# Performance work log

Hardware: AMD Instinct MI355X
Metric: run time of the kernel (lower is better)

The kernel has to match this reference:

```python
import jax, jax.numpy as jnp
import numpy as np


def setup_inputs() -> dict:
    key = jax.random.key(0)
    ks = jax.random.split(key, 8)
    n_videos, emb_dim = 200000, 128
    n_nodes, k_neigh = 20000, 32
    sc = 1.0 / np.sqrt(emb_dim)
    return {
        "video_embeddings": jax.random.normal(ks[0], (n_videos, emb_dim), jnp.float32),
        "video_nodes": jax.random.randint(ks[1], (n_nodes,), 0, n_videos, jnp.int64 if jax.config.jax_enable_x64 else jnp.int32),
        "neigh_idx": jax.random.randint(ks[2], (n_nodes, k_neigh), 0, n_videos, jnp.int64 if jax.config.jax_enable_x64 else jnp.int32),
        "W1": jax.random.normal(ks[3], (2 * emb_dim, emb_dim), jnp.float32) * sc,
        "b1": jnp.zeros((emb_dim,), jnp.float32),
        "W2": jax.random.normal(ks[4], (emb_dim, emb_dim), jnp.float32) * sc,
        "b2": jnp.zeros((emb_dim,), jnp.float32),
        "W3": jax.random.normal(ks[5], (emb_dim, 1), jnp.float32) * sc,
        "b3": jnp.zeros((1,), jnp.float32),
    }


def reference(video_embeddings, video_nodes, neigh_idx, W1, b1, W2, b2, W3, b3):
    # Ragged per-node loop vectorized as a padded [N, K] neighbor gather.
    neigh_emb = video_embeddings[neigh_idx]          # [N, K, D]
    node_emb = video_embeddings[video_nodes]         # [N, D]
    n, k, d = neigh_emb.shape
    # Attention MLP: cat(neigh, node_repeated) -> relu -> relu -> scalar score
    x = jnp.concatenate([neigh_emb, jnp.broadcast_to(node_emb[:, None, :], (n, k, d))], axis=-1)  # [N, K, 2D]
    h = jax.nn.relu(jnp.einsum("nke,ed->nkd", x, W1) + b1)
    h = jax.nn.relu(jnp.einsum("nke,ed->nkd", h, W2) + b2)
    scores = (jnp.einsum("nkd,do->nko", h, W3) + b3)[..., 0]  # [N, K]
    att = jax.nn.softmax(scores, axis=-1)                      # softmax over neighbors
    # Weighted aggregation: embed_matrix[i] = neigh_emb[i].T @ att[i]
    return jnp.einsum("nkd,nk->nd", neigh_emb, att)
```

## Files before the change

### kernel.cpp

```cpp
#include <hip/hip_runtime.h>
#include <hip/hip_bf16.h>

#define D  128
#define KN 32

typedef __attribute__((ext_vector_type(8))) short bf16x8;
typedef __attribute__((ext_vector_type(4))) float f32x4;

static __device__ __forceinline__ unsigned short f2bf(float f) {
    union { float f; unsigned int u; } v; v.f = f;
    unsigned int u = v.u;
    u += 0x7fff + ((u >> 16) & 1);
    return (unsigned short)(u >> 16);
}
static __device__ __forceinline__ float bf2f(unsigned short h) {
    union { float f; unsigned int u; } v; v.u = ((unsigned int)h) << 16;
    return v.f;
}

__global__ __launch_bounds__(256) void wt_kernel(
    const float* __restrict__ W1, const float* __restrict__ W2,
    unsigned short* __restrict__ W1Tt, unsigned short* __restrict__ W1Tb,
    unsigned short* __restrict__ W2T)
{
    int idx = blockIdx.x * 256 + threadIdx.x;
    if (idx < D * D) {
        int col = idx >> 7, e = idx & 127;
        W1Tt[col * D + e] = f2bf(W1[e * D + col]);
        W1Tb[col * D + e] = f2bf(W1[(D + e) * D + col]);
        W2T [col * D + e] = f2bf(W2[e * D + col]);
    }
}

__global__ __launch_bounds__(256) void p1q_kernel(
    const float* __restrict__ emb, const int* __restrict__ vnodes,
    int NV, int NN, int nvBlocks,
    const unsigned short* __restrict__ W1Tt, const unsigned short* __restrict__ W1Tb,
    const float* __restrict__ b1,
    unsigned short* __restrict__ P1, unsigned short* __restrict__ Q,
    unsigned short* __restrict__ EB)
{
    __shared__ unsigned short sA[128][136];

    const int tid  = threadIdx.x;
    const int lane = tid & 63;
    const int w    = tid >> 6;
    const int m    = lane & 15, q = lane >> 4;

    const bool nv = (int)blockIdx.x < nvBlocks;
    const int  bi = nv ? blockIdx.x : blockIdx.x - nvBlocks;
    const int  M  = nv ? NV : NN;
    const unsigned short* WT = nv ? W1Tt : W1Tb;
    unsigned short* dst = nv ? P1 : Q;
    const int r0 = bi * 128;

#pragma unroll
    for (int i = 0; i < 16; ++i) {
        int e = tid + 256 * i;
        int row = e >> 5, c4 = (e & 31) << 2;
        int r = r0 + row; if (r > M - 1) r = M - 1;
        int vr = nv ? r : vnodes[r];
        const float4 f = *(const float4*)(emb + (long)vr * D + c4);
        ushort4 h;
        h.x = f2bf(f.x); h.y = f2bf(f.y); h.z = f2bf(f.z); h.w = f2bf(f.w);
        *(ushort4*)(&sA[row][c4]) = h;
    }
    __syncthreads();

    if (nv) {
        int row = tid >> 1, half = tid & 1;
        if (r0 + row < M) {
#pragma unroll
            for (int j = 0; j < 8; ++j)
                *(bf16x8*)(EB + (long)(r0 + row) * D + half * 64 + j * 8) =
                    *(const bf16x8*)(&sA[row][half * 64 + j * 8]);
        }
    }

    bf16x8 Bf[2][4];
#pragma unroll
    for (int nt = 0; nt < 2; ++nt)
#pragma unroll
        for (int kk = 0; kk < 4; ++kk)
            Bf[nt][kk] = *(const bf16x8*)(WT + (32 * w + 16 * nt + m) * D + kk * 32 + q * 8);
    float bv[2];
#pragma unroll
    for (int nt = 0; nt < 2; ++nt) bv[nt] = nv ? 0.f : b1[32 * w + 16 * nt + m];

    f32x4 acc[8][2];
#pragma unroll
    for (int mt = 0; mt < 8; ++mt)
#pragma unroll
        for (int nt = 0; nt < 2; ++nt) acc[mt][nt] = (f32x4){0.f, 0.f, 0.f, 0.f};

#pragma unroll
    for (int kk = 0; kk < 4; ++kk) {
#pragma unroll
        for (int mt = 0; mt < 8; ++mt) {
            bf16x8 a = *(const bf16x8*)(&sA[16 * mt + m][kk * 32 + q * 8]);
            acc[mt][0] = __builtin_amdgcn_mfma_f32_16x16x32_bf16(a, Bf[0][kk], acc[mt][0], 0, 0, 0);
            acc[mt][1] = __builtin_amdgcn_mfma_f32_16x16x32_bf16(a, Bf[1][kk], acc[mt][1], 0, 0, 0);
        }
    }

#pragma unroll
    for (int mt = 0; mt < 8; ++mt)
#pragma unroll
        for (int nt = 0; nt < 2; ++nt) {
            int col = 32 * w + 16 * nt + m;
#pragma unroll
            for (int r = 0; r < 4; ++r) {
                int row = r0 + 16 * mt + 4 * q + r;
                if (row < M) dst[(long)row * D + col] = f2bf(acc[mt][nt][r] + bv[nt]);
            }
        }
}

__global__ __launch_bounds__(256, 2) void agg_kernel(
    const unsigned short* __restrict__ EB, const int* __restrict__ nidx,
    const unsigned short* __restrict__ W2T, const float* __restrict__ b2,
    const float* __restrict__ W3, const float* __restrict__ b3,
    const unsigned short* __restrict__ P1, const unsigned short* __restrict__ Q,
    float* __restrict__ out, int NN)
{
    __shared__ unsigned short sX[128][136];
    __shared__ int   sIdx[128];
    __shared__ float sSp[4][128];
    __shared__ float sAtt[128];

    const int tid  = threadIdx.x;
    const int lane = tid & 63;
    const int w    = tid >> 6;
    const int m    = lane & 15, q = lane >> 4;
    const int row  = tid >> 1, half = tid & 1;

    bf16x8 Bf[2][4];
#pragma unroll
    for (int nt = 0; nt < 2; ++nt)
#pragma unroll
        for (int kk = 0; kk < 4; ++kk)
            Bf[nt][kk] = *(const bf16x8*)(W2T + (32 * w + 16 * nt + m) * D + kk * 32 + q * 8);
    float b2v[2], w3v[2];
#pragma unroll
    for (int nt = 0; nt < 2; ++nt) {
        int col = 32 * w + 16 * nt + m;
        b2v[nt] = b2[col];
        w3v[nt] = W3[col];
    }
    const float b3s = b3[0];

    const int groups = (NN + 3) >> 2;

    int g = blockIdx.x;
    int ni_cur = 0;
    bf16x8 pf[8];
    if (g < groups) {
        int nd = g * 4 + (row >> 5); if (nd > NN - 1) nd = NN - 1;
        ni_cur = nidx[nd * KN + (row & 31)];
#pragma unroll
        for (int j = 0; j < 8; ++j)
            pf[j] = *(const bf16x8*)(P1 + (long)ni_cur * D + half * 64 + j * 8);
    }

    for (; g < groups; g += gridDim.x) {
        const int node0 = g * 4;
        int nd = node0 + (row >> 5); if (nd > NN - 1) nd = NN - 1;

        if (half == 0) sIdx[row] = ni_cur;
        {
            const bf16x8* qq = (const bf16x8*)(Q + (long)nd * D) + half * 8;
#pragma unroll
            for (int j = 0; j < 8; ++j) {
                bf16x8 qv = qq[j], r;
#pragma unroll
                for (int h = 0; h < 8; ++h) {
                    float v = bf2f((unsigned short)pf[j][h]) + bf2f((unsigned short)qv[h]);
                    r[h] = (short)f2bf(v > 0.f ? v : 0.f);
                }
                *(bf16x8*)(&sX[row][half * 64 + j * 8]) = r;
            }
        }

        const int gn = g + gridDim.x;
        const bool more = gn < groups;
        int ni_next = ni_cur;
        if (more) {
            int ndn = gn * 4 + (row >> 5); if (ndn > NN - 1) ndn = NN - 1;
            ni_next = nidx[ndn * KN + (row & 31)];
        }
        __syncthreads();

        bf16x8 gv[8];
#pragma unroll
        for (int j = 0; j < 8; ++j) {
            int k = (lane >> 4) + 4 * j;
            int ik = sIdx[w * KN + k];
            gv[j] = *(const bf16x8*)(EB + (long)ik * D + (lane & 15) * 8);
        }

        if (more) {
#pragma unroll
            for (int j = 0; j < 8; ++j)
                pf[j] = *(const bf16x8*)(P1 + (long)ni_next * D + half * 64 + j * 8);
        }

        f32x4 acc[8][2];
#pragma unroll
        for (int mt = 0; mt < 8; ++mt)
#pragma unroll
            for (int nt = 0; nt < 2; ++nt) acc[mt][nt] = (f32x4){0.f, 0.f, 0.f, 0.f};

#pragma unroll
        for (int kk = 0; kk < 4; ++kk) {
#pragma unroll
            for (int mt = 0; mt < 8; ++mt) {
                bf16x8 a = *(const bf16x8*)(&sX[16 * mt + m][kk * 32 + q * 8]);
                acc[mt][0] = __builtin_amdgcn_mfma_f32_16x16x32_bf16(a, Bf[0][kk], acc[mt][0], 0, 0, 0);
                acc[mt][1] = __builtin_amdgcn_mfma_f32_16x16x32_bf16(a, Bf[1][kk], acc[mt][1], 0, 0, 0);
            }
        }

#pragma unroll
        for (int mt = 0; mt < 8; ++mt) {
            float p[4];
#pragma unroll
            for (int r = 0; r < 4; ++r) {
                float h0 = acc[mt][0][r] + b2v[0]; h0 = h0 > 0.f ? h0 : 0.f;
                float h1 = acc[mt][1][r] + b2v[1]; h1 = h1 > 0.f ? h1 : 0.f;
                p[r] = h0 * w3v[0] + h1 * w3v[1];
            }
#pragma unroll
            for (int off = 8; off >= 1; off >>= 1)
#pragma unroll
                for (int r = 0; r < 4; ++r) p[r] += __shfl_xor(p[r], off, 16);
            if (m == 0) {
#pragma unroll
                for (int r = 0; r < 4; ++r) sSp[w][16 * mt + 4 * q + r] = p[r];
            }
        }
        __syncthreads();

        if (tid < 128) {
            float s = sSp[0][tid] + sSp[1][tid] + sSp[2][tid] + sSp[3][tid] + b3s;
            float mx = s;
#pragma unroll
            for (int off = 16; off >= 1; off >>= 1) mx = fmaxf(mx, __shfl_xor(mx, off, 32));
            float e = __expf(s - mx);
            float sum = e;
#pragma unroll
            for (int off = 16; off >= 1; off >>= 1) sum += __shfl_xor(sum, off, 32);
            sAtt[tid] = e / sum;
        }
        __syncthreads();

        {
            float r[8] = {0.f, 0.f, 0.f, 0.f, 0.f, 0.f, 0.f, 0.f};
#pragma unroll
            for (int j = 0; j < 8; ++j) {
                float a = sAtt[w * KN + (lane >> 4) + 4 * j];
#pragma unroll
                for (int h = 0; h < 8; ++h)
                    r[h] += a * bf2f((unsigned short)gv[j][h]);
            }
#pragma unroll
            for (int h = 0; h < 8; ++h) {
                r[h] += __shfl_xor(r[h], 16);
                r[h] += __shfl_xor(r[h], 32);
            }
            int ndw = node0 + w;
            if (lane < 16 && ndw < NN) {
                float4 o0 = {r[0], r[1], r[2], r[3]};
                float4 o1 = {r[4], r[5], r[6], r[7]};
                *(float4*)(out + (long)ndw * D + lane * 8)     = o0;
                *(float4*)(out + (long)ndw * D + lane * 8 + 4) = o1;
            }
        }
        ni_cur = ni_next;
    }
}

__global__ __launch_bounds__(128) void naive_kernel(
    const float* __restrict__ emb, const int* __restrict__ vnodes,
    const int* __restrict__ nidx,
    const float* __restrict__ W1, const float* __restrict__ b1,
    const float* __restrict__ W2, const float* __restrict__ b2,
    const float* __restrict__ W3, const float* __restrict__ b3,
    float* __restrict__ out)
{
    __shared__ float sE[KN + 1][D];
    __shared__ float sH[KN][D];
    __shared__ float sH2[KN][D];
    __shared__ float sS[KN];
    __shared__ float sA2[KN];
    const int node = blockIdx.x, tid = threadIdx.x;

    for (int r = 0; r < KN + 1; ++r) {
        int vr = (r < KN) ? nidx[node * KN + r] : vnodes[node];
        sE[r][tid] = emb[(long)vr * D + tid];
    }
    __syncthreads();
    for (int k = 0; k < KN; ++k) {
        float s = b1[tid];
        for (int e = 0; e < D; ++e) s += sE[k][e]  * W1[e * D + tid];
        for (int e = 0; e < D; ++e) s += sE[KN][e] * W1[(D + e) * D + tid];
        sH[k][tid] = s > 0.f ? s : 0.f;
    }
    __syncthreads();
    for (int k = 0; k < KN; ++k) {
        float s = b2[tid];
        for (int e = 0; e < D; ++e) s += sH[k][e] * W2[e * D + tid];
        sH2[k][tid] = s > 0.f ? s : 0.f;
    }
    __syncthreads();
    if (tid < KN) {
        float s = b3[0];
        for (int e = 0; e < D; ++e) s += sH2[tid][e] * W3[e];
        sS[tid] = s;
    }
    __syncthreads();
    if (tid == 0) {
        float mx = sS[0];
        for (int k = 1; k < KN; ++k) mx = fmaxf(mx, sS[k]);
        float sum = 0.f;
        for (int k = 0; k < KN; ++k) { sA2[k] = __expf(sS[k] - mx); sum += sA2[k]; }
        for (int k = 0; k < KN; ++k) sA2[k] /= sum;
    }
    __syncthreads();
    float a = 0.f;
    for (int k = 0; k < KN; ++k) a += sA2[k] * sE[k][tid];
    out[(long)node * D + tid] = a;
}

extern "C" void kernel_launch(void* const* d_in, const int* in_sizes, int n_in,
                              void* d_out, int out_size, void* d_ws, size_t ws_size,
                              hipStream_t stream) {
    const float* emb    = (const float*)d_in[0];
    const int*   vnodes = (const int*)d_in[1];
    const int*   nidx   = (const int*)d_in[2];
    const float* W1     = (const float*)d_in[3];
    const float* b1     = (const float*)d_in[4];
    const float* W2     = (const float*)d_in[5];
    const float* b2     = (const float*)d_in[6];
    const float* W3     = (const float*)d_in[7];
    const float* b3     = (const float*)d_in[8];
    float* out = (float*)d_out;

    const int NV = in_sizes[0] / D;
    const int NN = in_sizes[1];

    const size_t p1_elems = (size_t)NV * D;
    const size_t q_elems  = (size_t)NN * D;
    const size_t wt_elems = (size_t)D * D;
    const size_t need = (2 * p1_elems + q_elems + 3 * wt_elems) * sizeof(unsigned short);

    if (ws_size >= need) {
        unsigned short* P1   = (unsigned short*)d_ws;
        unsigned short* Q    = P1 + p1_elems;
        unsigned short* W1Tt = Q + q_elems;
        unsigned short* W1Tb = W1Tt + wt_elems;
        unsigned short* W2T  = W1Tb + wt_elems;
        unsigned short* EB   = W2T + wt_elems;

        const int nvBlocks = (NV + 127) / 128;
        const int qBlocks  = (NN + 127) / 128;

        wt_kernel<<<(D * D + 255) / 256, 256, 0, stream>>>(W1, W2, W1Tt, W1Tb, W2T);
        p1q_kernel<<<nvBlocks + qBlocks, 256, 0, stream>>>(
            emb, vnodes, NV, NN, nvBlocks, W1Tt, W1Tb, b1, P1, Q, EB);
        agg_kernel<<<1024, 256, 0, stream>>>(
            EB, nidx, W2T, b2, W3, b3, P1, Q, out, NN);
    } else {
        naive_kernel<<<NN, D, 0, stream>>>(emb, vnodes, nidx, W1, b1, W2, b2, W3, b3, out);
    }
}
```

Measured before the change: 302.7 us.

## Interleave P1 and bf16 embeddings per row, one-wave-per-node aggregation kernel

The precomputed W1 projection (P1) and the bf16 embedding copy now sit interleaved in a single 256-wide row, so each neighbour gather reads one contiguous 512-byte row instead of two separate buffers. The p1q output is staged through shared memory so global stores are coalesced. The aggregation kernel is restructured so each wave handles one node on its own: A fragments are built in registers, W2 lives in LDS, and scores and softmax are reduced with shuffles, which removes the block-wide barriers. Occupancy is raised to 4 blocks per SM, but the explicit prefetch of the next group's data is dropped.

Result: slower. 526.0 us (+73.8%).

```diff
diff --git a/kernel.cpp b/kernel.cpp
--- a/kernel.cpp
+++ b/kernel.cpp
@@ -37,8 +37,7 @@
     int NV, int NN, int nvBlocks,
     const unsigned short* __restrict__ W1Tt, const unsigned short* __restrict__ W1Tb,
     const float* __restrict__ b1,
-    unsigned short* __restrict__ P1, unsigned short* __restrict__ Q,
-    unsigned short* __restrict__ EB)
+    unsigned short* __restrict__ PE, unsigned short* __restrict__ Q)
 {
     __shared__ unsigned short sA[128][136];
 
@@ -51,7 +50,6 @@
     const int  bi = nv ? blockIdx.x : blockIdx.x - nvBlocks;
     const int  M  = nv ? NV : NN;
     const unsigned short* WT = nv ? W1Tt : W1Tb;
-    unsigned short* dst = nv ? P1 : Q;
     const int r0 = bi * 128;
 
 #pragma unroll
@@ -72,7 +70,7 @@
         if (r0 + row < M) {
 #pragma unroll
             for (int j = 0; j < 8; ++j)
-                *(bf16x8*)(EB + (long)(r0 + row) * D + half * 64 + j * 8) =
+                *(bf16x8*)(PE + (long)(r0 + row) * 256 + 128 + half * 64 + j * 8) =
                     *(const bf16x8*)(&sA[row][half * 64 + j * 8]);
         }
     }
@@ -103,179 +101,171 @@
         }
     }
 
+    __syncthreads();
 #pragma unroll
     for (int mt = 0; mt < 8; ++mt)
 #pragma unroll
         for (int nt = 0; nt < 2; ++nt) {
             int col = 32 * w + 16 * nt + m;
 #pragma unroll
-            for (int r = 0; r < 4; ++r) {
-                int row = r0 + 16 * mt + 4 * q + r;
-                if (row < M) dst[(long)row * D + col] = f2bf(acc[mt][nt][r] + bv[nt]);
+            for (int r = 0; r < 4; ++r)
+                sA[16 * mt + 4 * q + r][col] = f2bf(acc[mt][nt][r] + bv[nt]);
+        }
+    __syncthreads();
+    {
+        int row = tid >> 1, half = tid & 1;
+        int gr = r0 + row;
+        if (gr < M) {
+            if (nv) {
+#pragma unroll
+                for (int j = 0; j < 8; ++j)
+                    *(bf16x8*)(PE + (long)gr * 256 + half * 64 + j * 8) =
+                        *(const bf16x8*)(&sA[row][half * 64 + j * 8]);
+            } else {
+#pragma unroll
+                for (int j = 0; j < 8; ++j)
+                    *(bf16x8*)(Q + (long)gr * D + half * 64 + j * 8) =
+                        *(const bf16x8*)(&sA[row][half * 64 + j * 8]);
             }
         }
-}
-
-__global__ __launch_bounds__(256, 2) void agg_kernel(
-    const unsigned short* __restrict__ EB, const int* __restrict__ nidx,
+    }
+}
+
+__global__ __launch_bounds__(256, 4) void agg_kernel(
+    const unsigned short* __restrict__ PE, const int* __restrict__ nidx,
     const unsigned short* __restrict__ W2T, const float* __restrict__ b2,
     const float* __restrict__ W3, const float* __restrict__ b3,
-    const unsigned short* __restrict__ P1, const unsigned short* __restrict__ Q,
+    const unsigned short* __restrict__ Q,
     float* __restrict__ out, int NN)
 {
-    __shared__ unsigned short sX[128][136];
-    __shared__ int   sIdx[128];
-    __shared__ float sSp[4][128];
-    __shared__ float sAtt[128];
+    __shared__ bf16x8 sB[2048];
+    __shared__ float  sB2[D], sW3[D];
 
     const int tid  = threadIdx.x;
     const int lane = tid & 63;
     const int w    = tid >> 6;
     const int m    = lane & 15, q = lane >> 4;
-    const int row  = tid >> 1, half = tid & 1;
-
-    bf16x8 Bf[2][4];
-#pragma unroll
-    for (int nt = 0; nt < 2; ++nt)
-#pragma unroll
-        for (int kk = 0; kk < 4; ++kk)
-            Bf[nt][kk] = *(const bf16x8*)(W2T + (32 * w + 16 * nt + m) * D + kk * 32 + q * 8);
-    float b2v[2], w3v[2];
-#pragma unroll
-    for (int nt = 0; nt < 2; ++nt) {
-        int col = 32 * w + 16 * nt + m;
-        b2v[nt] = b2[col];
-        w3v[nt] = W3[col];
-    }
+
+#pragma unroll
+    for (int i = 0; i < 8; ++i) {
+        int f  = tid + 256 * i;
+        int fi = f >> 6, l = f & 63;
+        int kk = fi >> 3, nt = fi & 7;
+        sB[f] = *(const bf16x8*)(W2T + ((nt * 16 + (l & 15)) << 7) + kk * 32 + (l >> 4) * 8);
+    }
+    if (tid < D) { sB2[tid] = b2[tid]; sW3[tid] = W3[tid]; }
+    __syncthreads();
+
     const float b3s = b3[0];
-
-    const int groups = (NN + 3) >> 2;
-
-    int g = blockIdx.x;
-    int ni_cur = 0;
-    bf16x8 pf[8];
-    if (g < groups) {
-        int nd = g * 4 + (row >> 5); if (nd > NN - 1) nd = NN - 1;
-        ni_cur = nidx[nd * KN + (row & 31)];
-#pragma unroll
-        for (int j = 0; j < 8; ++j)
-            pf[j] = *(const bf16x8*)(P1 + (long)ni_cur * D + half * 64 + j * 8);
-    }
-
-    for (; g < groups; g += gridDim.x) {
-        const int node0 = g * 4;
-        int nd = node0 + (row >> 5); if (nd > NN - 1) nd = NN - 1;
-
-        if (half == 0) sIdx[row] = ni_cur;
-        {
-            const bf16x8* qq = (const bf16x8*)(Q + (long)nd * D) + half * 8;
-#pragma unroll
-            for (int j = 0; j < 8; ++j) {
-                bf16x8 qv = qq[j], r;
-#pragma unroll
-                for (int h = 0; h < 8; ++h) {
-                    float v = bf2f((unsigned short)pf[j][h]) + bf2f((unsigned short)qv[h]);
-                    r[h] = (short)f2bf(v > 0.f ? v : 0.f);
+    const int nwaves = gridDim.x << 2;
+
+    for (int node = (blockIdx.x << 2) + w; node < NN; node += nwaves) {
+        int iv = (lane < KN) ? nidx[node * KN + lane] : 0;
+        const int ik0 = __shfl(iv, m);
+        const int ik1 = __shfl(iv, 16 + m);
+
+        bf16x8 p0[4], p1[4], qv[4];
+        const unsigned short* prow0 = PE + (long)ik0 * 256 + q * 8;
+        const unsigned short* prow1 = PE + (long)ik1 * 256 + q * 8;
+        const unsigned short* qrow  = Q  + (long)node * D + q * 8;
+#pragma unroll
+        for (int kk = 0; kk < 4; ++kk) {
+            p0[kk] = *(const bf16x8*)(prow0 + kk * 32);
+            p1[kk] = *(const bf16x8*)(prow1 + kk * 32);
+            qv[kk] = *(const bf16x8*)(qrow  + kk * 32);
+        }
+
+        bf16x8 A0[4], A1[4];
+#pragma unroll
+        for (int kk = 0; kk < 4; ++kk) {
+#pragma unroll
+            for (int h = 0; h < 8; ++h) {
+                float qf = bf2f((unsigned short)qv[kk][h]);
+                float v0 = bf2f((unsigned short)p0[kk][h]) + qf;
+                float v1 = bf2f((unsigned short)p1[kk][h]) + qf;
+                A0[kk][h] = (short)f2bf(v0 > 0.f ? v0 : 0.f);
+                A1[kk][h] = (short)f2bf(v1 > 0.f ? v1 : 0.f);
+            }
+        }
+
+        f32x4 acc[2][8];
+#pragma unroll
+        for (int mt = 0; mt < 2; ++mt)
+#pragma unroll
+            for (int nt = 0; nt < 8; ++nt) acc[mt][nt] = (f32x4){0.f, 0.f, 0.f, 0.f};
+
+#pragma unroll
+        for (int kk = 0; kk < 4; ++kk) {
+#pragma unroll
+            for (int nt = 0; nt < 8; ++nt) {
+                bf16x8 b = sB[((kk << 3) + nt) * 64 + lane];
+                acc[0][nt] = __builtin_amdgcn_mfma_f32_16x16x32_bf16(A0[kk], b, acc[0][nt], 0, 0, 0);
+                acc[1][nt] = __builtin_amdgcn_mfma_f32_16x16x32_bf16(A1[kk], b, acc[1][nt], 0, 0, 0);
+            }
+        }
+
+        float s[2][4];
+#pragma unroll
+        for (int mt = 0; mt < 2; ++mt) {
+#pragma unroll
+            for (int r = 0; r < 4; ++r) s[mt][r] = 0.f;
+#pragma unroll
+            for (int nt = 0; nt < 8; ++nt) {
+                float bc = sB2[nt * 16 + m], wc = sW3[nt * 16 + m];
+#pragma unroll
+                for (int r = 0; r < 4; ++r) {
+                    float h = acc[mt][nt][r] + bc;
+                    s[mt][r] += (h > 0.f ? h : 0.f) * wc;
                 }
-                *(bf16x8*)(&sX[row][half * 64 + j * 8]) = r;
             }
-        }
-
-        const int gn = g + gridDim.x;
-        const bool more = gn < groups;
-        int ni_next = ni_cur;
-        if (more) {
-            int ndn = gn * 4 + (row >> 5); if (ndn > NN - 1) ndn = NN - 1;
-            ni_next = nidx[ndn * KN + (row & 31)];
-        }
-        __syncthreads();
+#pragma unroll
+            for (int off = 8; off >= 1; off >>= 1)
+#pragma unroll
+                for (int r = 0; r < 4; ++r) s[mt][r] += __shfl_xor(s[mt][r], off, 16);
+#pragma unroll
+            for (int r = 0; r < 4; ++r) s[mt][r] += b3s;
+        }
+        float mx = s[0][0];
+#pragma unroll
+        for (int mt = 0; mt < 2; ++mt)
+#pragma unroll
+            for (int r = 0; r < 4; ++r) mx = fmaxf(mx, s[mt][r]);
+        mx = fmaxf(mx, __shfl_xor(mx, 16));
+        mx = fmaxf(mx, __shfl_xor(mx, 32));
+        float e[2][4], sum = 0.f;
+#pragma unroll
+        for (int mt = 0; mt < 2; ++mt)
+#pragma unroll
+            for (int r = 0; r < 4; ++r) { e[mt][r] = __expf(s[mt][r] - mx); sum += e[mt][r]; }
+        sum += __shfl_xor(sum, 16);
+        sum += __shfl_xor(sum, 32);
+        const float inv = 1.f / sum;
 
         bf16x8 gv[8];
 #pragma unroll
         for (int j = 0; j < 8; ++j) {
-            int k = (lane >> 4) + 4 * j;
-            int ik = sIdx[w * KN + k];
-            gv[j] = *(const bf16x8*)(EB + (long)ik * D + (lane & 15) * 8);
-        }
-
-        if (more) {
-#pragma unroll
-            for (int j = 0; j < 8; ++j)
-                pf[j] = *(const bf16x8*)(P1 + (long)ni_next * D + half * 64 + j * 8);
-        }
-
-        f32x4 acc[8][2];
-#pragma unroll
-        for (int mt = 0; mt < 8; ++mt)
-#pragma unroll
-            for (int nt = 0; nt < 2; ++nt) acc[mt][nt] = (f32x4){0.f, 0.f, 0.f, 0.f};
-
-#pragma unroll
-        for (int kk = 0; kk < 4; ++kk) {
-#pragma unroll
-            for (int mt = 0; mt < 8; ++mt) {
-                bf16x8 a = *(const bf16x8*)(&sX[16 * mt + m][kk * 32 + q * 8]);
-                acc[mt][0] = __builtin_amdgcn_mfma_f32_16x16x32_bf16(a, Bf[0][kk], acc[mt][0], 0, 0, 0);
-                acc[mt][1] = __builtin_amdgcn_mfma_f32_16x16x32_bf16(a, Bf[1][kk], acc[mt][1], 0, 0, 0);
-            }
-        }
-
-#pragma unroll
-        for (int mt = 0; mt < 8; ++mt) {
-            float p[4];
-#pragma unroll
-            for (int r = 0; r < 4; ++r) {
-                float h0 = acc[mt][0][r] + b2v[0]; h0 = h0 > 0.f ? h0 : 0.f;
-                float h1 = acc[mt][1][r] + b2v[1]; h1 = h1 > 0.f ? h1 : 0.f;
-                p[r] = h0 * w3v[0] + h1 * w3v[1];
-            }
-#pragma unroll
-            for (int off = 8; off >= 1; off >>= 1)
-#pragma unroll
-                for (int r = 0; r < 4; ++r) p[r] += __shfl_xor(p[r], off, 16);
-            if (m == 0) {
-#pragma unroll
-                for (int r = 0; r < 4; ++r) sSp[w][16 * mt + 4 * q + r] = p[r];
-            }
-        }
-        __syncthreads();
-
-        if (tid < 128) {
-            float s = sSp[0][tid] + sSp[1][tid] + sSp[2][tid] + sSp[3][tid] + b3s;
-            float mx = s;
-#pragma unroll
-            for (int off = 16; off >= 1; off >>= 1) mx = fmaxf(mx, __shfl_xor(mx, off, 32));
-            float e = __expf(s - mx);
-            float sum = e;
-#pragma unroll
-            for (int off = 16; off >= 1; off >>= 1) sum += __shfl_xor(sum, off, 32);
-            sAtt[tid] = e / sum;
-        }
-        __syncthreads();
-
-        {
-            float r[8] = {0.f, 0.f, 0.f, 0.f, 0.f, 0.f, 0.f, 0.f};
-#pragma unroll
-            for (int j = 0; j < 8; ++j) {
-                float a = sAtt[w * KN + (lane >> 4) + 4 * j];
-#pragma unroll
-                for (int h = 0; h < 8; ++h)
-                    r[h] += a * bf2f((unsigned short)gv[j][h]);
-            }
-#pragma unroll
-            for (int h = 0; h < 8; ++h) {
-                r[h] += __shfl_xor(r[h], 16);
-                r[h] += __shfl_xor(r[h], 32);
-            }
-            int ndw = node0 + w;
-            if (lane < 16 && ndw < NN) {
-                float4 o0 = {r[0], r[1], r[2], r[3]};
-                float4 o1 = {r[4], r[5], r[6], r[7]};
-                *(float4*)(out + (long)ndw * D + lane * 8)     = o0;
-                *(float4*)(out + (long)ndw * D + lane * 8 + 4) = o1;
-            }
-        }
-        ni_cur = ni_next;
+            int kj  = 4 * q + (j & 3) + 16 * (j >> 2);
+            int ikj = __shfl(iv, kj);
+            gv[j] = *(const bf16x8*)(PE + (long)ikj * 256 + 128 + m * 8);
+        }
+        float r8[8] = {0.f, 0.f, 0.f, 0.f, 0.f, 0.f, 0.f, 0.f};
+#pragma unroll
+        for (int j = 0; j < 8; ++j) {
+            float a = e[j >> 2][j & 3] * inv;
+#pragma unroll
+            for (int h = 0; h < 8; ++h) r8[h] += a * bf2f((unsigned short)gv[j][h]);
+        }
+#pragma unroll
+        for (int h = 0; h < 8; ++h) {
+            r8[h] += __shfl_xor(r8[h], 16);
+            r8[h] += __shfl_xor(r8[h], 32);
+        }
+        if (lane < 16) {
+            float4 o0 = {r8[0], r8[1], r8[2], r8[3]};
+            float4 o1 = {r8[4], r8[5], r8[6], r8[7]};
+            *(float4*)(out + (long)node * D + m * 8)     = o0;
+            *(float4*)(out + (long)node * D + m * 8 + 4) = o1;
+        }
     }
 }
 
@@ -348,27 +338,26 @@
     const int NV = in_sizes[0] / D;
     const int NN = in_sizes[1];
 
-    const size_t p1_elems = (size_t)NV * D;
+    const size_t pe_elems = (size_t)NV * 256;
     const size_t q_elems  = (size_t)NN * D;
     const size_t wt_elems = (size_t)D * D;
-    const size_t need = (2 * p1_elems + q_elems + 3 * wt_elems) * sizeof(unsigned short);
+    const size_t need = (pe_elems + q_elems + 3 * wt_elems) * sizeof(unsigned short);
 
     if (ws_size >= need) {
-        unsigned short* P1   = (unsigned short*)d_ws;
-        unsigned short* Q    = P1 + p1_elems;
+        unsigned short* PE   = (unsigned short*)d_ws;
+        unsigned short* Q    = PE + pe_elems;
         unsigned short* W1Tt = Q + q_elems;
         unsigned short* W1Tb = W1Tt + wt_elems;
         unsigned short* W2T  = W1Tb + wt_elems;
-        unsigned short* EB   = W2T + wt_elems;
 
         const int nvBlocks = (NV + 127) / 128;
         const int qBlocks  = (NN + 127) / 128;
 
         wt_kernel<<<(D * D + 255) / 256, 256, 0, stream>>>(W1, W2, W1Tt, W1Tb, W2T);
         p1q_kernel<<<nvBlocks + qBlocks, 256, 0, stream>>>(
-            emb, vnodes, NV, NN, nvBlocks, W1Tt, W1Tb, b1, P1, Q, EB);
+            emb, vnodes, NV, NN, nvBlocks, W1Tt, W1Tb, b1, PE, Q);
         agg_kernel<<<1024, 256, 0, stream>>>(
-            EB, nidx, W2T, b2, W3, b3, P1, Q, out, NN);
+            PE, nidx, W2T, b2, W3, b3, Q, out, NN);
     } else {
         naive_kernel<<<NN, D, 0, stream>>>(emb, vnodes, nidx, W1, b1, W2, b2, W3, b3, out);
     }
```

## Compute first MLP layer per gathered neighbor instead of precomputing for all videos

Applied to the files above, without the earlier changes.

The old code ran the W1-top GEMM over all 200k videos to build a P1 table, then gathered P1 rows per neighbor. The new code only converts embeddings to bf16 and computes the neighbor layer-1 product on the fly inside a per-node wave kernel. That kernel keeps W1/W2 fragments in shared memory, shuffles the layer-1 output into MFMA B-operand layout, and does the softmax and aggregation with wave shuffles instead of block syncs. This avoids GEMM work and P1 traffic for unreferenced videos (640k gathered rows against 200k table rows), at the cost of more MFMA work per node and heavier shuffle use. Q is now kept in fp32.

Result: slower. 458.0 us (+51.3%).

```diff
diff --git a/kernel.cpp b/kernel.cpp
--- a/kernel.cpp
+++ b/kernel.cpp
@@ -6,6 +6,8 @@
 
 typedef __attribute__((ext_vector_type(8))) short bf16x8;
 typedef __attribute__((ext_vector_type(4))) float f32x4;
+
+union bfu { bf16x8 v; unsigned int u[4]; };
 
 static __device__ __forceinline__ unsigned short f2bf(float f) {
     union { float f; unsigned int u; } v; v.f = f;
@@ -32,250 +34,311 @@
     }
 }
 
-__global__ __launch_bounds__(256) void p1q_kernel(
+__global__ __launch_bounds__(256) void ebq_kernel(
     const float* __restrict__ emb, const int* __restrict__ vnodes,
-    int NV, int NN, int nvBlocks,
-    const unsigned short* __restrict__ W1Tt, const unsigned short* __restrict__ W1Tb,
-    const float* __restrict__ b1,
-    unsigned short* __restrict__ P1, unsigned short* __restrict__ Q,
-    unsigned short* __restrict__ EB)
+    int NV, int NN, int ebBlocks,
+    const unsigned short* __restrict__ W1Tb, const float* __restrict__ b1,
+    unsigned short* __restrict__ EB, float* __restrict__ Qf)
 {
     __shared__ unsigned short sA[128][136];
+    const int tid = threadIdx.x;
+
+    if ((int)blockIdx.x < ebBlocks) {
+        const long base  = (long)blockIdx.x * 16384;
+        const long total = (long)NV * D;
+#pragma unroll
+        for (int j = 0; j < 8; ++j) {
+            long p = base + j * 2048 + tid * 8;
+            if (p < total) {
+                float4 f0 = *(const float4*)(emb + p);
+                float4 f1 = *(const float4*)(emb + p + 4);
+                bf16x8 o;
+                o[0] = (short)f2bf(f0.x); o[1] = (short)f2bf(f0.y);
+                o[2] = (short)f2bf(f0.z); o[3] = (short)f2bf(f0.w);
+                o[4] = (short)f2bf(f1.x); o[5] = (short)f2bf(f1.y);
+                o[6] = (short)f2bf(f1.z); o[7] = (short)f2bf(f1.w);
+                *(bf16x8*)(EB + p) = o;
+            }
+        }
+        return;
+    }
+
+    const int bi   = blockIdx.x - ebBlocks;
+    const int lane = tid & 63;
+    const int w    = tid >> 6;
+    const int m    = lane & 15, q = lane >> 4;
+    const int r0   = bi * 128;
+
+#pragma unroll
+    for (int i = 0; i < 16; ++i) {
+        int e = tid + 256 * i;
+        int row = e >> 5, c4 = (e & 31) << 2;
+        int r = r0 + row; if (r > NN - 1) r = NN - 1;
+        int vr = vnodes[r];
+        const float4 f = *(const float4*)(emb + (long)vr * D + c4);
+        ushort4 h;
+        h.x = f2bf(f.x); h.y = f2bf(f.y); h.z = f2bf(f.z); h.w = f2bf(f.w);
+        *(ushort4*)(&sA[row][c4]) = h;
+    }
+    __syncthreads();
+
+    bf16x8 Bf[2][4];
+#pragma unroll
+    for (int nt = 0; nt < 2; ++nt)
+#pragma unroll
+        for (int kk = 0; kk < 4; ++kk)
+            Bf[nt][kk] = *(const bf16x8*)(W1Tb + (32 * w + 16 * nt + m) * D + kk * 32 + q * 8);
+    float bv[2];
+#pragma unroll
+    for (int nt = 0; nt < 2; ++nt) bv[nt] = b1[32 * w + 16 * nt + m];
+
+    f32x4 acc[8][2];
+#pragma unroll
+    for (int mt = 0; mt < 8; ++mt)
+#pragma unroll
+        for (int nt = 0; nt < 2; ++nt) acc[mt][nt] = (f32x4){0.f, 0.f, 0.f, 0.f};
+
+#pragma unroll
+    for (int kk = 0; kk < 4; ++kk) {
+#pragma unroll
+        for (int mt = 0; mt < 8; ++mt) {
+            bf16x8 a = *(const bf16x8*)(&sA[16 * mt + m][kk * 32 + q * 8]);
+            acc[mt][0] = __builtin_amdgcn_mfma_f32_16x16x32_bf16(a, Bf[0][kk], acc[mt][0], 0, 0, 0);
+            acc[mt][1] = __builtin_amdgcn_mfma_f32_16x16x32_bf16(a, Bf[1][kk], acc[mt][1], 0, 0, 0);
+        }
+    }
+
+#pragma unroll
+    for (int mt = 0; mt < 8; ++mt)
+#pragma unroll
+        for (int nt = 0; nt < 2; ++nt) {
+            int col = 32 * w + 16 * nt + m;
+#pragma unroll
+            for (int r = 0; r < 4; ++r) {
+                int row = r0 + 16 * mt + 4 * q + r;
+                if (row < NN) Qf[(long)row * D + col] = acc[mt][nt][r] + bv[nt];
+            }
+        }
+}
+
+__global__ __launch_bounds__(256, 2) void node_kernel(
+    const unsigned short* __restrict__ EB, const int* __restrict__ nidx,
+    const float* __restrict__ Qf,
+    const unsigned short* __restrict__ W1Tt, const unsigned short* __restrict__ W2T,
+    const float* __restrict__ b2, const float* __restrict__ W3,
+    const float* __restrict__ b3,
+    float* __restrict__ out, int NN)
+{
+    __shared__ bf16x8 sA1[2048];
+    __shared__ bf16x8 sA2[2048];
+    __shared__ float  sb2f[128], sw3f[128];
 
     const int tid  = threadIdx.x;
     const int lane = tid & 63;
     const int w    = tid >> 6;
     const int m    = lane & 15, q = lane >> 4;
 
-    const bool nv = (int)blockIdx.x < nvBlocks;
-    const int  bi = nv ? blockIdx.x : blockIdx.x - nvBlocks;
-    const int  M  = nv ? NV : NN;
-    const unsigned short* WT = nv ? W1Tt : W1Tb;
-    unsigned short* dst = nv ? P1 : Q;
-    const int r0 = bi * 128;
-
-#pragma unroll
-    for (int i = 0; i < 16; ++i) {
-        int e = tid + 256 * i;
-        int row = e >> 5, c4 = (e & 31) << 2;
-        int r = r0 + row; if (r > M - 1) r = M - 1;
-        int vr = nv ? r : vnodes[r];
-        const float4 f = *(const float4*)(emb + (long)vr * D + c4);
-        ushort4 h;
-        h.x = f2bf(f.x); h.y = f2bf(f.y); h.z = f2bf(f.z); h.w = f2bf(f.w);
-        *(ushort4*)(&sA[row][c4]) = h;
-    }
-    __syncthreads();
-
-    if (nv) {
-        int row = tid >> 1, half = tid & 1;
-        if (r0 + row < M) {
-#pragma unroll
-            for (int j = 0; j < 8; ++j)
-                *(bf16x8*)(EB + (long)(r0 + row) * D + half * 64 + j * 8) =
-                    *(const bf16x8*)(&sA[row][half * 64 + j * 8]);
-        }
-    }
-
-    bf16x8 Bf[2][4];
-#pragma unroll
-    for (int nt = 0; nt < 2; ++nt)
+#pragma unroll
+    for (int i = 0; i < 8; ++i) {
+        int f  = tid + 256 * i;
+        int fi = f >> 6, l = f & 63;
+        int kk = fi >> 3, mt = fi & 7;
+        int off = ((16 * mt + (l & 15)) << 7) + kk * 32 + (l >> 4) * 8;
+        sA1[f] = *(const bf16x8*)(W1Tt + off);
+        sA2[f] = *(const bf16x8*)(W2T + off);
+    }
+    if (tid < 128) { sb2f[tid] = b2[tid]; sw3f[tid] = W3[tid]; }
+    __syncthreads();
+
+    const float b3s = b3[0];
+    const int stride = gridDim.x << 2;
+    int node = (blockIdx.x << 2) + w;
+    if (node >= NN) return;
+
+    bf16x8 ebC[2][4], ebN[2][4];
+    {
+        int iv = (lane < KN) ? nidx[node * KN + lane] : 0;
+        const long i0 = __shfl(iv, m);
+        const long i1 = __shfl(iv, 16 + m);
+        const unsigned short* p0 = EB + i0 * D + q * 8;
+        const unsigned short* p1 = EB + i1 * D + q * 8;
+#pragma unroll
+        for (int kk = 0; kk < 4; ++kk) {
+            ebC[0][kk] = *(const bf16x8*)(p0 + kk * 32);
+            ebC[1][kk] = *(const bf16x8*)(p1 + kk * 32);
+        }
+    }
+
+    for (; node < NN; node += stride) {
+        f32x4 qv[8];
+#pragma unroll
+        for (int mt = 0; mt < 8; ++mt)
+            qv[mt] = *(const f32x4*)(Qf + (long)node * D + 16 * mt + 4 * q);
+
+        const int noden = node + stride;
+        const bool more = noden < NN;
+        int ivn = (more && lane < KN) ? nidx[noden * KN + lane] : 0;
+
+        f32x4 acc1[8][2];
+#pragma unroll
+        for (int mt = 0; mt < 8; ++mt) {
+            acc1[mt][0] = (f32x4){0.f, 0.f, 0.f, 0.f};
+            acc1[mt][1] = (f32x4){0.f, 0.f, 0.f, 0.f};
+        }
 #pragma unroll
         for (int kk = 0; kk < 4; ++kk)
-            Bf[nt][kk] = *(const bf16x8*)(WT + (32 * w + 16 * nt + m) * D + kk * 32 + q * 8);
-    float bv[2];
-#pragma unroll
-    for (int nt = 0; nt < 2; ++nt) bv[nt] = nv ? 0.f : b1[32 * w + 16 * nt + m];
-
-    f32x4 acc[8][2];
-#pragma unroll
-    for (int mt = 0; mt < 8; ++mt)
-#pragma unroll
-        for (int nt = 0; nt < 2; ++nt) acc[mt][nt] = (f32x4){0.f, 0.f, 0.f, 0.f};
-
-#pragma unroll
-    for (int kk = 0; kk < 4; ++kk) {
+#pragma unroll
+            for (int mt = 0; mt < 8; ++mt) {
+                bf16x8 a = sA1[((kk << 3) + mt) * 64 + lane];
+                acc1[mt][0] = __builtin_amdgcn_mfma_f32_16x16x32_bf16(a, ebC[0][kk], acc1[mt][0], 0, 0, 0);
+                acc1[mt][1] = __builtin_amdgcn_mfma_f32_16x16x32_bf16(a, ebC[1][kk], acc1[mt][1], 0, 0, 0);
+            }
+
+        unsigned int hp[8][2][2];
+#pragma unroll
+        for (int mt = 0; mt < 8; ++mt)
+#pragma unroll
+            for (int nt = 0; nt < 2; ++nt) {
+                float v0 = acc1[mt][nt][0] + qv[mt][0]; v0 = v0 > 0.f ? v0 : 0.f;
+                float v1 = acc1[mt][nt][1] + qv[mt][1]; v1 = v1 > 0.f ? v1 : 0.f;
+                float v2 = acc1[mt][nt][2] + qv[mt][2]; v2 = v2 > 0.f ? v2 : 0.f;
+                float v3 = acc1[mt][nt][3] + qv[mt][3]; v3 = v3 > 0.f ? v3 : 0.f;
+                hp[mt][nt][0] = (unsigned)f2bf(v0) | ((unsigned)f2bf(v1) << 16);
+                hp[mt][nt][1] = (unsigned)f2bf(v2) | ((unsigned)f2bf(v3) << 16);
+            }
+
+        const int srcLo = ((q & 1) << 5) + m;
+        const int srcHi = srcLo + 16;
+        const bool hiSel = (q & 2) != 0;
+        bfu B2[2][4];
+#pragma unroll
+        for (int nt = 0; nt < 2; ++nt)
+#pragma unroll
+            for (int kk = 0; kk < 4; ++kk) {
+                unsigned aa0 = __shfl(hp[2 * kk][nt][0], srcLo);
+                unsigned bb0 = __shfl(hp[2 * kk + 1][nt][0], srcLo);
+                unsigned aa1 = __shfl(hp[2 * kk][nt][1], srcLo);
+                unsigned bb1 = __shfl(hp[2 * kk + 1][nt][1], srcLo);
+                unsigned cc0 = __shfl(hp[2 * kk][nt][0], srcHi);
+                unsigned dd0 = __shfl(hp[2 * kk + 1][nt][0], srcHi);
+                unsigned cc1 = __shfl(hp[2 * kk][nt][1], srcHi);
+                unsigned dd1 = __shfl(hp[2 * kk + 1][nt][1], srcHi);
+                B2[nt][kk].u[0] = hiSel ? bb0 : aa0;
+                B2[nt][kk].u[1] = hiSel ? bb1 : aa1;
+                B2[nt][kk].u[2] = hiSel ? dd0 : cc0;
+                B2[nt][kk].u[3] = hiSel ? dd1 : cc1;
+            }
+
+        if (more) {
+            const long i0 = __shfl(ivn, m);
+            const long i1 = __shfl(ivn, 16 + m);
+            const unsigned short* p0 = EB + i0 * D + q * 8;
+            const unsigned short* p1 = EB + i1 * D + q * 8;
+#pragma unroll
+            for (int kk = 0; kk < 4; ++kk) {
+                ebN[0][kk] = *(const bf16x8*)(p0 + kk * 32);
+                ebN[1][kk] = *(const bf16x8*)(p1 + kk * 32);
+            }
+        }
+
+        f32x4 acc2[8][2];
 #pragma unroll
         for (int mt = 0; mt < 8; ++mt) {
-            bf16x8 a = *(const bf16x8*)(&sA[16 * mt + m][kk * 32 + q * 8]);
-            acc[mt][0] = __builtin_amdgcn_mfma_f32_16x16x32_bf16(a, Bf[0][kk], acc[mt][0], 0, 0, 0);
-            acc[mt][1] = __builtin_amdgcn_mfma_f32_16x16x32_bf16(a, Bf[1][kk], acc[mt][1], 0, 0, 0);
-        }
-    }
-
-#pragma unroll
-    for (int mt = 0; mt < 8; ++mt)
-#pragma unroll
-        for (int nt = 0; nt < 2; ++nt) {
-            int col = 32 * w + 16 * nt + m;
+            acc2[mt][0] = (f32x4){0.f, 0.f, 0.f, 0.f};
+            acc2[mt][1] = (f32x4){0.f, 0.f, 0.f, 0.f};
+        }
+#pragma unroll
+        for (int kk = 0; kk < 4; ++kk)
+#pragma unroll
+            for (int mt = 0; mt < 8; ++mt) {
+                bf16x8 a = sA2[((kk << 3) + mt) * 64 + lane];
+                acc2[mt][0] = __builtin_amdgcn_mfma_f32_16x16x32_bf16(a, B2[0][kk].v, acc2[mt][0], 0, 0, 0);
+                acc2[mt][1] = __builtin_amdgcn_mfma_f32_16x16x32_bf16(a, B2[1][kk].v, acc2[mt][1], 0, 0, 0);
+            }
+
+        float sp0 = 0.f, sp1 = 0.f;
+#pragma unroll
+        for (int mt = 0; mt < 8; ++mt) {
+            f32x4 bb = *(const f32x4*)(&sb2f[16 * mt + 4 * q]);
+            f32x4 ww = *(const f32x4*)(&sw3f[16 * mt + 4 * q]);
 #pragma unroll
             for (int r = 0; r < 4; ++r) {
-                int row = r0 + 16 * mt + 4 * q + r;
-                if (row < M) dst[(long)row * D + col] = f2bf(acc[mt][nt][r] + bv[nt]);
-            }
-        }
-}
-
-__global__ __launch_bounds__(256, 2) void agg_kernel(
-    const unsigned short* __restrict__ EB, const int* __restrict__ nidx,
-    const unsigned short* __restrict__ W2T, const float* __restrict__ b2,
-    const float* __restrict__ W3, const float* __restrict__ b3,
-    const unsigned short* __restrict__ P1, const unsigned short* __restrict__ Q,
-    float* __restrict__ out, int NN)
-{
-    __shared__ unsigned short sX[128][136];
-    __shared__ int   sIdx[128];
-    __shared__ float sSp[4][128];
-    __shared__ float sAtt[128];
-
-    const int tid  = threadIdx.x;
-    const int lane = tid & 63;
-    const int w    = tid >> 6;
-    const int m    = lane & 15, q = lane >> 4;
-    const int row  = tid >> 1, half = tid & 1;
-
-    bf16x8 Bf[2][4];
-#pragma unroll
-    for (int nt = 0; nt < 2; ++nt)
+                float h0 = acc2[mt][0][r] + bb[r]; h0 = h0 > 0.f ? h0 : 0.f;
+                float h1 = acc2[mt][1][r] + bb[r]; h1 = h1 > 0.f ? h1 : 0.f;
+                sp0 += h0 * ww[r];
+                sp1 += h1 * ww[r];
+            }
+        }
+        sp0 += __shfl_xor(sp0, 16); sp0 += __shfl_xor(sp0, 32);
+        sp1 += __shfl_xor(sp1, 16); sp1 += __shfl_xor(sp1, 32);
+        const float s0 = sp0 + b3s, s1 = sp1 + b3s;
+
+        float mx = fmaxf(s0, s1);
+#pragma unroll
+        for (int off = 1; off <= 8; off <<= 1) mx = fmaxf(mx, __shfl_xor(mx, off));
+        float e0v = __expf(s0 - mx), e1v = __expf(s1 - mx);
+        float sum = e0v + e1v;
+#pragma unroll
+        for (int off = 1; off <= 8; off <<= 1) sum += __shfl_xor(sum, off);
+        const float inv  = 1.f / sum;
+        const float att0 = e0v * inv, att1 = e1v * inv;
+
+        float pa[32];
 #pragma unroll
         for (int kk = 0; kk < 4; ++kk)
-            Bf[nt][kk] = *(const bf16x8*)(W2T + (32 * w + 16 * nt + m) * D + kk * 32 + q * 8);
-    float b2v[2], w3v[2];
-#pragma unroll
-    for (int nt = 0; nt < 2; ++nt) {
-        int col = 32 * w + 16 * nt + m;
-        b2v[nt] = b2[col];
-        w3v[nt] = W3[col];
-    }
-    const float b3s = b3[0];
-
-    const int groups = (NN + 3) >> 2;
-
-    int g = blockIdx.x;
-    int ni_cur = 0;
-    bf16x8 pf[8];
-    if (g < groups) {
-        int nd = g * 4 + (row >> 5); if (nd > NN - 1) nd = NN - 1;
-        ni_cur = nidx[nd * KN + (row & 31)];
-#pragma unroll
-        for (int j = 0; j < 8; ++j)
-            pf[j] = *(const bf16x8*)(P1 + (long)ni_cur * D + half * 64 + j * 8);
-    }
-
-    for (; g < groups; g += gridDim.x) {
-        const int node0 = g * 4;
-        int nd = node0 + (row >> 5); if (nd > NN - 1) nd = NN - 1;
-
-        if (half == 0) sIdx[row] = ni_cur;
+#pragma unroll
+            for (int h = 0; h < 8; ++h)
+                pa[kk * 8 + h] = att0 * bf2f((unsigned short)ebC[0][kk][h])
+                               + att1 * bf2f((unsigned short)ebC[1][kk][h]);
+
         {
-            const bf16x8* qq = (const bf16x8*)(Q + (long)nd * D) + half * 8;
+            const bool hi = (m & 8) != 0;
+#pragma unroll
+            for (int j = 0; j < 16; ++j) {
+                float sv = hi ? pa[j] : pa[16 + j];
+                float rv = __shfl_xor(sv, 8);
+                pa[j] = (hi ? pa[16 + j] : pa[j]) + rv;
+            }
+        }
+        {
+            const bool hi = (m & 4) != 0;
 #pragma unroll
             for (int j = 0; j < 8; ++j) {
-                bf16x8 qv = qq[j], r;
-#pragma unroll
-                for (int h = 0; h < 8; ++h) {
-                    float v = bf2f((unsigned short)pf[j][h]) + bf2f((unsigned short)qv[h]);
-                    r[h] = (short)f2bf(v > 0.f ? v : 0.f);
-                }
-                *(bf16x8*)(&sX[row][half * 64 + j * 8]) = r;
-            }
-        }
-
-        const int gn = g + gridDim.x;
-        const bool more = gn < groups;
-        int ni_next = ni_cur;
+                float sv = hi ? pa[j] : pa[8 + j];
+                float rv = __shfl_xor(sv, 4);
+                pa[j] = (hi ? pa[8 + j] : pa[j]) + rv;
+            }
+        }
+        {
+            const bool hi = (m & 2) != 0;
+#pragma unroll
+            for (int j = 0; j < 4; ++j) {
+                float sv = hi ? pa[j] : pa[4 + j];
+                float rv = __shfl_xor(sv, 2);
+                pa[j] = (hi ? pa[4 + j] : pa[j]) + rv;
+            }
+        }
+        {
+            const bool hi = (m & 1) != 0;
+#pragma unroll
+            for (int j = 0; j < 2; ++j) {
+                float sv = hi ? pa[j] : pa[2 + j];
+                float rv = __shfl_xor(sv, 1);
+                pa[j] = (hi ? pa[2 + j] : pa[j]) + rv;
+            }
+        }
+        {
+            int e0 = ((m >> 2) << 5) + (q << 3) + ((m & 3) << 1);
+            float2 o; o.x = pa[0]; o.y = pa[1];
+            *(float2*)(out + (long)node * D + e0) = o;
+        }
+
         if (more) {
-            int ndn = gn * 4 + (row >> 5); if (ndn > NN - 1) ndn = NN - 1;
-            ni_next = nidx[ndn * KN + (row & 31)];
-        }
-        __syncthreads();
-
-        bf16x8 gv[8];
-#pragma unroll
-        for (int j = 0; j < 8; ++j) {
-            int k = (lane >> 4) + 4 * j;
-            int ik = sIdx[w * KN + k];
-            gv[j] = *(const bf16x8*)(EB + (long)ik * D + (lane & 15) * 8);
-        }
-
-        if (more) {
-#pragma unroll
-            for (int j = 0; j < 8; ++j)
-                pf[j] = *(const bf16x8*)(P1 + (long)ni_next * D + half * 64 + j * 8);
-        }
-
-        f32x4 acc[8][2];
-#pragma unroll
-        for (int mt = 0; mt < 8; ++mt)
-#pragma unroll
-            for (int nt = 0; nt < 2; ++nt) acc[mt][nt] = (f32x4){0.f, 0.f, 0.f, 0.f};
-
-#pragma unroll
-        for (int kk = 0; kk < 4; ++kk) {
-#pragma unroll
-            for (int mt = 0; mt < 8; ++mt) {
-                bf16x8 a = *(const bf16x8*)(&sX[16 * mt + m][kk * 32 + q * 8]);
-                acc[mt][0] = __builtin_amdgcn_mfma_f32_16x16x32_bf16(a, Bf[0][kk], acc[mt][0], 0, 0, 0);
-                acc[mt][1] = __builtin_amdgcn_mfma_f32_16x16x32_bf16(a, Bf[1][kk], acc[mt][1], 0, 0, 0);
-            }
-        }
-
-#pragma unroll
-        for (int mt = 0; mt < 8; ++mt) {
-            float p[4];
-#pragma unroll
-            for (int r = 0; r < 4; ++r) {
-                float h0 = acc[mt][0][r] + b2v[0]; h0 = h0 > 0.f ? h0 : 0.f;
-                float h1 = acc[mt][1][r] + b2v[1]; h1 = h1 > 0.f ? h1 : 0.f;
-                p[r] = h0 * w3v[0] + h1 * w3v[1];
-            }
-#pragma unroll
-            for (int off = 8; off >= 1; off >>= 1)
-#pragma unroll
-                for (int r = 0; r < 4; ++r) p[r] += __shfl_xor(p[r], off, 16);
-            if (m == 0) {
-#pragma unroll
-                for (int r = 0; r < 4; ++r) sSp[w][16 * mt + 4 * q + r] = p[r];
-            }
-        }
-        __syncthreads();
-
-        if (tid < 128) {
-            float s = sSp[0][tid] + sSp[1][tid] + sSp[2][tid] + sSp[3][tid] + b3s;
-            float mx = s;
-#pragma unroll
-            for (int off = 16; off >= 1; off >>= 1) mx = fmaxf(mx, __shfl_xor(mx, off, 32));
-            float e = __expf(s - mx);
-            float sum = e;
-#pragma unroll
-            for (int off = 16; off >= 1; off >>= 1) sum += __shfl_xor(sum, off, 32);
-            sAtt[tid] = e / sum;
-        }
-        __syncthreads();
-
-        {
-            float r[8] = {0.f, 0.f, 0.f, 0.f, 0.f, 0.f, 0.f, 0.f};
-#pragma unroll
-            for (int j = 0; j < 8; ++j) {
-                float a = sAtt[w * KN + (lane >> 4) + 4 * j];
-#pragma unroll
-                for (int h = 0; h < 8; ++h)
-                    r[h] += a * bf2f((unsigned short)gv[j][h]);
-            }
-#pragma unroll
-            for (int h = 0; h < 8; ++h) {
-                r[h] += __shfl_xor(r[h], 16);
-                r[h] += __shfl_xor(r[h], 32);
-            }
-            int ndw = node0 + w;
-            if (lane < 16 && ndw < NN) {
-                float4 o0 = {r[0], r[1], r[2], r[3]};
-                float4 o1 = {r[4], r[5], r[6], r[7]};
-                *(float4*)(out + (long)ndw * D + lane * 8)     = o0;
-                *(float4*)(out + (long)ndw * D + lane * 8 + 4) = o1;
-            }
-        }
-        ni_cur = ni_next;
+#pragma unroll
+            for (int nt = 0; nt < 2; ++nt)
+#pragma unroll
+                for (int kk = 0; kk < 4; ++kk) ebC[nt][kk] = ebN[nt][kk];
+        }
     }
 }
 
@@ -348,27 +411,27 @@
     const int NV = in_sizes[0] / D;
     const int NN = in_sizes[1];
 
-    const size_t p1_elems = (size_t)NV * D;
-    const size_t q_elems  = (size_t)NN * D;
-    const size_t wt_elems = (size_t)D * D;
-    const size_t need = (2 * p1_elems + q_elems + 3 * wt_elems) * sizeof(unsigned short);
+    const size_t q_bytes  = (size_t)NN * D * sizeof(float);
+    const size_t eb_bytes = (size_t)NV * D * sizeof(unsigned short);
+    const size_t wt_bytes = (size_t)D * D * sizeof(unsigned short);
+    const size_t need = q_bytes + eb_bytes + 3 * wt_bytes;
 
     if (ws_size >= need) {
-        unsigned short* P1   = (unsigned short*)d_ws;
-        unsigned short* Q    = P1 + p1_elems;
-        unsigned short* W1Tt = Q + q_elems;
-        unsigned short* W1Tb = W1Tt + wt_elems;
-        unsigned short* W2T  = W1Tb + wt_elems;
-        unsigned short* EB   = W2T + wt_elems;
-
-        const int nvBlocks = (NV + 127) / 128;
+        float*          Qf   = (float*)d_ws;
+        unsigned short* EB   = (unsigned short*)((char*)d_ws + q_bytes);
+        unsigned short* W1Tt = EB + (size_t)NV * D;
+        unsigned short* W1Tb = W1Tt + (size_t)D * D;
+        unsigned short* W2T  = W1Tb + (size_t)D * D;
+
+        const long total = (long)NV * D;
+        const int ebBlocks = (int)((total + 16383) / 16384);
         const int qBlocks  = (NN + 127) / 128;
 
         wt_kernel<<<(D * D + 255) / 256, 256, 0, stream>>>(W1, W2, W1Tt, W1Tb, W2T);
-        p1q_kernel<<<nvBlocks + qBlocks, 256, 0, stream>>>(
-            emb, vnodes, NV, NN, nvBlocks, W1Tt, W1Tb, b1, P1, Q, EB);
-        agg_kernel<<<1024, 256, 0, stream>>>(
-            EB, nidx, W2T, b2, W3, b3, P1, Q, out, NN);
+        ebq_kernel<<<ebBlocks + qBlocks, 256, 0, stream>>>(
+            emb, vnodes, NV, NN, ebBlocks, W1Tb, b1, EB, Qf);
+        node_kernel<<<512, 256, 0, stream>>>(
+            EB, nidx, Qf, W1Tt, W2T, b2, W3, b3, out, NN);
     } else {
         naive_kernel<<<NN, D, 0, stream>>>(emb, vnodes, nidx, W1, b1, W2, b2, W3, b3, out);
     }
```
